# Performance work log

Hardware: AMD Instinct MI355X
Metric: run time of the kernel (lower is better)

## Reference

```python
import jax, jax.numpy as jnp
import numpy as np

E, K, H, I = 8, 2, 1024, 3584  # num_experts, top_k, hidden, intermediate


def setup_inputs() -> dict:
    key = jax.random.key(0)
    k0, k1, k2, k3, k4 = jax.random.split(key, 5)
    scale = 0.02
    return {
        "hidden_states": jax.random.normal(k0, (2, 1024, H), dtype=jnp.float32),
        "w_gate": jax.random.normal(k1, (E, H), dtype=jnp.float32) * scale,  # gate Linear H->E
        "w1": jax.random.normal(k2, (E, I, H), dtype=jnp.float32) * scale,   # gate proj
        "w3": jax.random.normal(k3, (E, I, H), dtype=jnp.float32) * scale,   # up proj
        "w2": jax.random.normal(k4, (E, H, I), dtype=jnp.float32) * scale,   # down proj
    }


def reference(hidden_states, w_gate, w1, w3, w2):
    B, S, Hd = hidden_states.shape
    x = hidden_states.reshape(-1, Hd)                       # [T, H]
    logits = jnp.einsum('th,eh->te', x, w_gate)             # router logits [T, E]
    probs = jax.nn.softmax(logits, axis=-1)
    topw, topi = jax.lax.top_k(probs, K)                    # [T, K]
    topw = topw / jnp.sum(topw, axis=-1, keepdims=True)     # renormalize=True
    # dense combine weights [T, E] (zero off the top-k)
    comb = jnp.sum(jax.nn.one_hot(topi, E, dtype=x.dtype) * topw[..., None], axis=1)
    # SwiGLU experts (dense reference over all experts; math matches dispatch+combine)
    g = jnp.einsum('th,eih->eti', x, w1)                    # [E, T, I]
    u = jnp.einsum('th,eih->eti', x, w3)
    h = jax.nn.silu(g) * u
    out = jnp.einsum('eti,ehi->eth', h, w2)                 # [E, T, H]
    y = jnp.einsum('te,eth->th', comb, out)                 # weighted combine
    return y.reshape(B, S, Hd)
```

## Files before the change

kernel.cpp:

```cpp
#include <hip/hip_runtime.h>
#include <hip/hip_bf16.h>
#include <stdint.h>

#define NEXP 8
#define HD 1024
#define ID 3584
#define NTOK 2048
#define NSLOT 4096
#define SLOT_PAD 128
#define NSLOT_ALLOC (NSLOT + SLOT_PAD)
#define WN (NEXP * ID * HD)
#define KSPLIT 4
#define KLEN (ID / KSPLIT)

typedef unsigned short u16;
typedef __attribute__((ext_vector_type(8))) short s16x8;
typedef __attribute__((ext_vector_type(4))) short s16x4;
typedef __attribute__((ext_vector_type(4))) float f32x4;

__device__ __forceinline__ u16 f2bf(float f) {
    __hip_bfloat16 h = __float2bfloat16(f);
    union { __hip_bfloat16 h; u16 u; } v; v.h = h; return v.u;
}

__device__ __forceinline__ s16x8 cvt8(f32x4 a, f32x4 b) {
    s16x8 o;
    o[0]=(short)f2bf(a[0]); o[1]=(short)f2bf(a[1]); o[2]=(short)f2bf(a[2]); o[3]=(short)f2bf(a[3]);
    o[4]=(short)f2bf(b[0]); o[5]=(short)f2bf(b[1]); o[6]=(short)f2bf(b[2]); o[7]=(short)f2bf(b[3]);
    return o;
}

__device__ __forceinline__ void glds16(const void* g, void* l) {
    __builtin_amdgcn_global_load_lds((const __attribute__((address_space(1))) unsigned*)g,
                                     (__attribute__((address_space(3))) unsigned*)l, 16, 0, 0);
}

__global__ void init_kernel(int* __restrict__ counts) {
    if (threadIdx.x < 16) counts[threadIdx.x] = 0;
}

__global__ void router_kernel(const float* __restrict__ x, const float* __restrict__ wg,
                              int* __restrict__ topk_idx, float* __restrict__ topk_w,
                              int* __restrict__ counts) {
    int t = blockIdx.x;
    int lane = threadIdx.x;
    const float* xr = x + (size_t)t * HD;
    float acc[NEXP];
#pragma unroll
    for (int e = 0; e < NEXP; ++e) acc[e] = 0.f;
#pragma unroll
    for (int i = 0; i < HD / 256; ++i) {
        int h = i * 256 + lane * 4;
        f32x4 xv = *(const f32x4*)(xr + h);
#pragma unroll
        for (int e = 0; e < NEXP; ++e) {
            f32x4 wv = *(const f32x4*)(wg + e * HD + h);
            acc[e] += xv[0]*wv[0] + xv[1]*wv[1] + xv[2]*wv[2] + xv[3]*wv[3];
        }
    }
#pragma unroll
    for (int e = 0; e < NEXP; ++e) {
#pragma unroll
        for (int s = 32; s > 0; s >>= 1) acc[e] += __shfl_xor(acc[e], s, 64);
    }
    if (lane == 0) {
        int b0 = 0; float l0 = acc[0];
#pragma unroll
        for (int e = 1; e < NEXP; ++e) if (acc[e] > l0) { l0 = acc[e]; b0 = e; }
        int b1 = (b0 == 0) ? 1 : 0; float l1 = acc[b1];
#pragma unroll
        for (int e = 0; e < NEXP; ++e) {
            if (e == b0 || e == b1) continue;
            if (acc[e] > l1) { l1 = acc[e]; b1 = e; }
        }
        float w0 = 1.f / (1.f + expf(l1 - l0));
        float w1 = 1.f - w0;
        topk_idx[2 * t] = b0; topk_idx[2 * t + 1] = b1;
        topk_w[2 * t] = w0;  topk_w[2 * t + 1] = w1;
        atomicAdd(&counts[b0], 1);
        atomicAdd(&counts[b1], 1);
    }
}

__global__ void scan_kernel(const int* __restrict__ counts, int* __restrict__ offsets,
                            int* __restrict__ rows) {
    if (threadIdx.x == 0) {
        int off = 0;
#pragma unroll
        for (int e = 0; e < NEXP; ++e) { offsets[e] = off; off += counts[e]; }
    }
    if (threadIdx.x < SLOT_PAD) rows[NSLOT + threadIdx.x] = 0;
}

__global__ void assign_kernel(const int* __restrict__ topk_idx, const int* __restrict__ offsets,
                              int* __restrict__ counts2, int* __restrict__ rows,
                              int* __restrict__ slot_of) {
    int i = blockIdx.x * 256 + threadIdx.x;
    int e = topk_idx[i];
    int pos = atomicAdd(&counts2[e], 1);
    int slot = offsets[e] + pos;
    rows[slot] = i >> 1;
    slot_of[i] = slot;
}

__global__ __launch_bounds__(256)
void cvt3_kernel(const float* __restrict__ x, u16* __restrict__ xbf,
                 const float* __restrict__ w1, u16* __restrict__ w1bf,
                 const float* __restrict__ w3, u16* __restrict__ w3bf) {
    const int NX = NTOK * HD / 8, NW = WN / 8;
    int stride = gridDim.x * 256;
    for (int i = blockIdx.x * 256 + threadIdx.x; i < NX + 2 * NW; i += stride) {
        const float* s; u16* d; int j;
        if (i < NX)            { s = x;  d = xbf;  j = i; }
        else if (i < NX + NW)  { s = w1; d = w1bf; j = i - NX; }
        else                   { s = w3; d = w3bf; j = i - NX - NW; }
        f32x4 v0 = ((const f32x4*)s)[2 * j];
        f32x4 v1 = ((const f32x4*)s)[2 * j + 1];
        ((s16x8*)d)[j] = cvt8(v0, v1);
    }
}

#define G1_BLOCKS (NEXP * (NTOK / 128) * (ID / 128))
#define CVT2_BLOCKS 1024
__global__ __launch_bounds__(256, 2)
void gemm1_kernel(const u16* __restrict__ xbf, const u16* __restrict__ w1bf,
                  const u16* __restrict__ w3bf, const int* __restrict__ counts,
                  const int* __restrict__ offsets, const int* __restrict__ rows,
                  u16* __restrict__ hbuf,
                  const float* __restrict__ w2, u16* __restrict__ w2bf) {
    __shared__ u16 As[128][32];
    __shared__ u16 B1s[128][32];
    __shared__ u16 B3s[128][32];

    if (blockIdx.x >= G1_BLOCKS) {
        const int stride = CVT2_BLOCKS * 256;
        for (int i = (blockIdx.x - G1_BLOCKS) * 256 + threadIdx.x; i < WN / 8; i += stride) {
            f32x4 v0 = ((const f32x4*)w2)[2 * i];
            f32x4 v1 = ((const f32x4*)w2)[2 * i + 1];
            ((s16x8*)w2bf)[i] = cvt8(v0, v1);
        }
        return;
    }

    int bid = blockIdx.x;
    int gq = bid >> 7;
    int rm = bid & 127;
    int mt = rm >> 3;
    int g  = gq * 8 + (rm & 7);
    int e  = g / 28;
    int nt = g - e * 28;

    int n_e = counts[e];
    int m0 = mt * 128;
    if (m0 >= n_e) return;
    int off = offsets[e];
    int n0 = nt * 128;

    int tid = threadIdx.x;
    int lane = tid & 63;
    int wid = tid >> 6;

    int srow = wid * 32 + (lane >> 2);
    int chunk = ((lane & 3) ^ ((srow >> 1) & 3)) * 8;

    int tokA0 = rows[off + m0 + srow];
    int tokA1 = rows[off + m0 + srow + 16];
    const u16* srcA0 = xbf + (size_t)tokA0 * HD + chunk;
    const u16* srcA1 = xbf + (size_t)tokA1 * HD + chunk;
    const u16* srcB1a = w1bf + ((size_t)e * ID + n0 + srow) * HD + chunk;
    const u16* srcB1b = srcB1a + (size_t)16 * HD;
    const u16* srcB3a = w3bf + ((size_t)e * ID + n0 + srow) * HD + chunk;
    const u16* srcB3b = srcB3a + (size_t)16 * HD;

    f32x4 accg[4][4] = {}, accu[4][4] = {};
    int wm = (wid >> 1) * 64, wn = (wid & 1) * 64;
    int lr = lane & 15;
    int k8sw = ((lane >> 4) ^ ((lr >> 1) & 3)) * 8;

    for (int k0 = 0; k0 < HD; k0 += 32) {
        glds16(srcA0 + k0,  &As[wid * 32][0]);
        glds16(srcA1 + k0,  &As[wid * 32 + 16][0]);
        glds16(srcB1a + k0, &B1s[wid * 32][0]);
        glds16(srcB1b + k0, &B1s[wid * 32 + 16][0]);
        glds16(srcB3a + k0, &B3s[wid * 32][0]);
        glds16(srcB3b + k0, &B3s[wid * 32 + 16][0]);
        __syncthreads();
        s16x8 a[4], b1[4], b3[4];
#pragma unroll
        for (int f = 0; f < 4; ++f) {
            a[f]  = *(const s16x8*)&As[wm + f * 16 + lr][k8sw];
            b1[f] = *(const s16x8*)&B1s[wn + f * 16 + lr][k8sw];
            b3[f] = *(const s16x8*)&B3s[wn + f * 16 + lr][k8sw];
        }
#pragma unroll
        for (int fm = 0; fm < 4; ++fm)
#pragma unroll
            for (int fn = 0; fn < 4; ++fn) {
                accg[fm][fn] = __builtin_amdgcn_mfma_f32_16x16x32_bf16(a[fm], b1[fn], accg[fm][fn], 0, 0, 0);
                accu[fm][fn] = __builtin_amdgcn_mfma_f32_16x16x32_bf16(a[fm], b3[fn], accu[fm][fn], 0, 0, 0);
            }
        __syncthreads();
    }

    int lc = lane & 15;
    int lr4 = (lane >> 4) * 4;
#pragma unroll
    for (int fm = 0; fm < 4; ++fm) {
#pragma unroll
        for (int r = 0; r < 4; ++r) {
            int row = wm + fm * 16 + lr4 + r;
            if (m0 + row < n_e) {
                size_t base = (size_t)(off + m0 + row) * ID + n0 + wn;
#pragma unroll
                for (int fn = 0; fn < 4; ++fn) {
                    float g2 = accg[fm][fn][r];
                    float u = accu[fm][fn][r];
                    float hv = g2 * u / (1.f + expf(-g2));
                    hbuf[base + fn * 16 + lc] = f2bf(hv);
                }
            }
        }
    }
}

__global__ __launch_bounds__(256, 2)
void gemm2_kernel(const u16* __restrict__ hbuf, const u16* __restrict__ w2bf,
                  const int* __restrict__ counts, const int* __restrict__ offsets,
                  float* __restrict__ out2) {
    int bid = blockIdx.x;
    int e = bid & 7;
    int inner = bid >> 3;
    int mt = inner >> 5;
    int r2 = inner & 31;
    int nt = r2 >> 2;
    int ks = r2 & 3;

    int n_e = counts[e];
    int m0 = mt * 128;
    if (m0 >= n_e) return;
    int off = offsets[e];
    int n0 = nt * 128;
    int kbase = ks * KLEN;

    __shared__ u16 As[128][32];
    __shared__ u16 Bs[128][32];

    int tid = threadIdx.x;
    int lane = tid & 63;
    int wid = tid >> 6;

    int srow = wid * 32 + (lane >> 2);
    int chunk = ((lane & 3) ^ ((srow >> 1) & 3)) * 8;
    const u16* srcA0 = hbuf + (size_t)(off + m0 + srow) * ID + kbase + chunk;
    const u16* srcA1 = srcA0 + (size_t)16 * ID;
    const u16* srcB0 = w2bf + ((size_t)e * HD + n0 + srow) * ID + kbase + chunk;
    const u16* srcB1 = srcB0 + (size_t)16 * ID;

    f32x4 acc[4][4] = {};
    int wm = (wid >> 1) * 64, wn = (wid & 1) * 64;
    int lr = lane & 15;
    int k8sw = ((lane >> 4) ^ ((lr >> 1) & 3)) * 8;

    for (int k0 = 0; k0 < KLEN; k0 += 32) {
        glds16(srcA0 + k0, &As[wid * 32][0]);
        glds16(srcA1 + k0, &As[wid * 32 + 16][0]);
        glds16(srcB0 + k0, &Bs[wid * 32][0]);
        glds16(srcB1 + k0, &Bs[wid * 32 + 16][0]);
        __syncthreads();
        s16x8 a[4], b[4];
#pragma unroll
        for (int f = 0; f < 4; ++f) {
            a[f] = *(const s16x8*)&As[wm + f * 16 + lr][k8sw];
            b[f] = *(const s16x8*)&Bs[wn + f * 16 + lr][k8sw];
        }
#pragma unroll
        for (int fm = 0; fm < 4; ++fm)
#pragma unroll
            for (int fn = 0; fn < 4; ++fn)
                acc[fm][fn] = __builtin_amdgcn_mfma_f32_16x16x32_bf16(a[fm], b[fn], acc[fm][fn], 0, 0, 0);
        __syncthreads();
    }

    float* outp = out2 + (size_t)ks * NSLOT_ALLOC * HD;
    int lc = lane & 15;
    int lr4 = (lane >> 4) * 4;
#pragma unroll
    for (int fm = 0; fm < 4; ++fm) {
#pragma unroll
        for (int r = 0; r < 4; ++r) {
            int row = wm + fm * 16 + lr4 + r;
            if (m0 + row < n_e) {
                float* dst = outp + (size_t)(off + m0 + row) * HD + n0 + wn;
#pragma unroll
                for (int fn = 0; fn < 4; ++fn)
                    dst[fn * 16 + lc] = acc[fm][fn][r];
            }
        }
    }
}

__global__ void combine_kernel(const float* __restrict__ out2, const int* __restrict__ slot_of,
                               const float* __restrict__ topk_w, float* __restrict__ y) {
    int i = blockIdx.x * 256 + threadIdx.x;
    int t = i >> 8;
    int c = i & 255;
    int s0 = slot_of[2 * t], s1 = slot_of[2 * t + 1];
    float w0 = topk_w[2 * t], w1 = topk_w[2 * t + 1];
    f32x4 o = {0.f, 0.f, 0.f, 0.f};
#pragma unroll
    for (int ks = 0; ks < KSPLIT; ++ks) {
        const float* p = out2 + (size_t)ks * NSLOT_ALLOC * HD;
        f32x4 a = ((const f32x4*)(p + (size_t)s0 * HD))[c];
        f32x4 b = ((const f32x4*)(p + (size_t)s1 * HD))[c];
#pragma unroll
        for (int j = 0; j < 4; ++j) o[j] += w0 * a[j] + w1 * b[j];
    }
    ((f32x4*)(y + (size_t)t * HD))[c] = o;
}

extern "C" void kernel_launch(void* const* d_in, const int* in_sizes, int n_in,
                              void* d_out, int out_size, void* d_ws, size_t ws_size,
                              hipStream_t stream) {
    (void)in_sizes; (void)n_in; (void)out_size; (void)ws_size;
    const float* x  = (const float*)d_in[0];
    const float* wg = (const float*)d_in[1];
    const float* w1 = (const float*)d_in[2];
    const float* w3 = (const float*)d_in[3];
    const float* w2 = (const float*)d_in[4];
    float* y = (float*)d_out;

    char* ws = (char*)d_ws;
    int*   counts   = (int*)(ws + 0);
    int*   counts2  = (int*)(ws + 32);
    int*   offsets  = (int*)(ws + 64);
    int*   topk_idx = (int*)(ws + 128);
    float* topk_w   = (float*)(ws + 128 + (size_t)NSLOT * 4);
    int*   rows     = (int*)(ws + 128 + (size_t)NSLOT * 8);
    int*   slot_of  = (int*)(ws + 128 + (size_t)NSLOT * 8 + (size_t)NSLOT_ALLOC * 4);
    size_t off_xbf = 128 + (size_t)NSLOT * 12 + (size_t)NSLOT_ALLOC * 4;
    off_xbf = (off_xbf + 255) & ~(size_t)255;
    u16* xbf = (u16*)(ws + off_xbf);
    size_t off_h = off_xbf + (size_t)NTOK * HD * 2;
    u16* hbuf = (u16*)(ws + off_h);
    size_t off_w1 = off_h + (size_t)NSLOT_ALLOC * ID * 2;
    u16* w1bf = (u16*)(ws + off_w1);
    size_t off_w3 = off_w1 + (size_t)WN * 2;
    u16* w3bf = (u16*)(ws + off_w3);
    size_t off_w2 = off_w3 + (size_t)WN * 2;
    u16* w2bf = (u16*)(ws + off_w2);
    size_t off_o2 = off_w2 + (size_t)WN * 2;
    float* out2 = (float*)(ws + off_o2);

    init_kernel<<<1, 64, 0, stream>>>(counts);
    router_kernel<<<NTOK, 64, 0, stream>>>(x, wg, topk_idx, topk_w, counts);
    scan_kernel<<<1, 128, 0, stream>>>(counts, offsets, rows);
    assign_kernel<<<NSLOT / 256, 256, 0, stream>>>(topk_idx, offsets, counts2, rows, slot_of);
    cvt3_kernel<<<4096, 256, 0, stream>>>(x, xbf, w1, w1bf, w3, w3bf);
    gemm1_kernel<<<G1_BLOCKS + CVT2_BLOCKS, 256, 0, stream>>>(xbf, w1bf, w3bf, counts, offsets, rows, hbuf, w2, w2bf);
    gemm2_kernel<<<NEXP * (NTOK / 128) * (HD / 128) * KSPLIT, 256, 0, stream>>>(hbuf, w2bf, counts, offsets, out2);
    combine_kernel<<<(NTOK * HD / 4) / 256, 256, 0, stream>>>(out2, slot_of, topk_w, y);
}
```

Baseline: 345.2 us.

## Double K-tile depth to 64 in both expert GEMMs with 8-way XOR swizzle

Raises the K step of each LDS tile from 32 to 64 in gemm1 and gemm2. Each stage now issues four 16-byte global-to-LDS loads per row group and runs two MFMA sub-steps per sync, with the swizzle changed to an 8-chunk XOR pattern. The aim is to halve the number of barriers and loop iterations per tile and amortize load latency. The cost is double the LDS per block, which may reduce occupancy, especially for gemm1 with its three tiles. Slot padding and scan block size are also raised to keep the rows array consistent with the new loading pattern.

```diff
diff --git a/kernel.cpp b/kernel.cpp
--- a/kernel.cpp
+++ b/kernel.cpp
@@ -7,7 +7,7 @@
 #define ID 3584
 #define NTOK 2048
 #define NSLOT 4096
-#define SLOT_PAD 128
+#define SLOT_PAD 256
 #define NSLOT_ALLOC (NSLOT + SLOT_PAD)
 #define WN (NEXP * ID * HD)
 #define KSPLIT 4
@@ -128,9 +128,9 @@
                   const int* __restrict__ offsets, const int* __restrict__ rows,
                   u16* __restrict__ hbuf,
                   const float* __restrict__ w2, u16* __restrict__ w2bf) {
-    __shared__ u16 As[128][32];
-    __shared__ u16 B1s[128][32];
-    __shared__ u16 B3s[128][32];
+    __shared__ u16 As[128][64];
+    __shared__ u16 B1s[128][64];
+    __shared__ u16 B3s[128][64];
 
     if (blockIdx.x >= G1_BLOCKS) {
         const int stride = CVT2_BLOCKS * 256;
@@ -160,37 +160,54 @@
     int lane = tid & 63;
     int wid = tid >> 6;
 
-    int srow = wid * 32 + (lane >> 2);
-    int chunk = ((lane & 3) ^ ((srow >> 1) & 3)) * 8;
-
-    int tokA0 = rows[off + m0 + srow];
-    int tokA1 = rows[off + m0 + srow + 16];
-    const u16* srcA0 = xbf + (size_t)tokA0 * HD + chunk;
-    const u16* srcA1 = xbf + (size_t)tokA1 * HD + chunk;
-    const u16* srcB1a = w1bf + ((size_t)e * ID + n0 + srow) * HD + chunk;
-    const u16* srcB1b = srcB1a + (size_t)16 * HD;
-    const u16* srcB3a = w3bf + ((size_t)e * ID + n0 + srow) * HD + chunk;
-    const u16* srcB3b = srcB3a + (size_t)16 * HD;
+    int rsub = lane >> 3;
+    int chunk = ((lane & 7) ^ rsub) * 8;
+    int srow = wid * 32 + rsub;
+
+    const u16 *srcA[4], *srcB1[4], *srcB3[4];
+#pragma unroll
+    for (int j = 0; j < 4; ++j) {
+        int rl = srow + 8 * j;
+        int tok = rows[off + m0 + rl];
+        srcA[j]  = xbf  + (size_t)tok * HD + chunk;
+        srcB1[j] = w1bf + ((size_t)e * ID + n0 + rl) * HD + chunk;
+        srcB3[j] = w3bf + ((size_t)e * ID + n0 + rl) * HD + chunk;
+    }
 
     f32x4 accg[4][4] = {}, accu[4][4] = {};
     int wm = (wid >> 1) * 64, wn = (wid & 1) * 64;
     int lr = lane & 15;
-    int k8sw = ((lane >> 4) ^ ((lr >> 1) & 3)) * 8;
-
-    for (int k0 = 0; k0 < HD; k0 += 32) {
-        glds16(srcA0 + k0,  &As[wid * 32][0]);
-        glds16(srcA1 + k0,  &As[wid * 32 + 16][0]);
-        glds16(srcB1a + k0, &B1s[wid * 32][0]);
-        glds16(srcB1b + k0, &B1s[wid * 32 + 16][0]);
-        glds16(srcB3a + k0, &B3s[wid * 32][0]);
-        glds16(srcB3b + k0, &B3s[wid * 32 + 16][0]);
+    int kk = lane >> 4;
+    int ks0 = ((kk)     ^ (lr & 7)) * 8;
+    int ks1 = ((4 + kk) ^ (lr & 7)) * 8;
+
+    for (int k0 = 0; k0 < HD; k0 += 64) {
+#pragma unroll
+        for (int j = 0; j < 4; ++j) {
+            glds16(srcA[j]  + k0, &As[wid * 32 + 8 * j][0]);
+            glds16(srcB1[j] + k0, &B1s[wid * 32 + 8 * j][0]);
+            glds16(srcB3[j] + k0, &B3s[wid * 32 + 8 * j][0]);
+        }
         __syncthreads();
         s16x8 a[4], b1[4], b3[4];
 #pragma unroll
         for (int f = 0; f < 4; ++f) {
-            a[f]  = *(const s16x8*)&As[wm + f * 16 + lr][k8sw];
-            b1[f] = *(const s16x8*)&B1s[wn + f * 16 + lr][k8sw];
-            b3[f] = *(const s16x8*)&B3s[wn + f * 16 + lr][k8sw];
+            a[f]  = *(const s16x8*)&As[wm + f * 16 + lr][ks0];
+            b1[f] = *(const s16x8*)&B1s[wn + f * 16 + lr][ks0];
+            b3[f] = *(const s16x8*)&B3s[wn + f * 16 + lr][ks0];
+        }
+#pragma unroll
+        for (int fm = 0; fm < 4; ++fm)
+#pragma unroll
+            for (int fn = 0; fn < 4; ++fn) {
+                accg[fm][fn] = __builtin_amdgcn_mfma_f32_16x16x32_bf16(a[fm], b1[fn], accg[fm][fn], 0, 0, 0);
+                accu[fm][fn] = __builtin_amdgcn_mfma_f32_16x16x32_bf16(a[fm], b3[fn], accu[fm][fn], 0, 0, 0);
+            }
+#pragma unroll
+        for (int f = 0; f < 4; ++f) {
+            a[f]  = *(const s16x8*)&As[wm + f * 16 + lr][ks1];
+            b1[f] = *(const s16x8*)&B1s[wn + f * 16 + lr][ks1];
+            b3[f] = *(const s16x8*)&B3s[wn + f * 16 + lr][ks1];
         }
 #pragma unroll
         for (int fm = 0; fm < 4; ++fm)
@@ -242,36 +259,54 @@
     int n0 = nt * 128;
     int kbase = ks * KLEN;
 
-    __shared__ u16 As[128][32];
-    __shared__ u16 Bs[128][32];
+    __shared__ u16 As[128][64];
+    __shared__ u16 Bs[128][64];
 
     int tid = threadIdx.x;
     int lane = tid & 63;
     int wid = tid >> 6;
 
-    int srow = wid * 32 + (lane >> 2);
-    int chunk = ((lane & 3) ^ ((srow >> 1) & 3)) * 8;
-    const u16* srcA0 = hbuf + (size_t)(off + m0 + srow) * ID + kbase + chunk;
-    const u16* srcA1 = srcA0 + (size_t)16 * ID;
-    const u16* srcB0 = w2bf + ((size_t)e * HD + n0 + srow) * ID + kbase + chunk;
-    const u16* srcB1 = srcB0 + (size_t)16 * ID;
+    int rsub = lane >> 3;
+    int chunk = ((lane & 7) ^ rsub) * 8;
+    int srow = wid * 32 + rsub;
+
+    const u16 *srcA[4], *srcB[4];
+#pragma unroll
+    for (int j = 0; j < 4; ++j) {
+        int rl = srow + 8 * j;
+        srcA[j] = hbuf + (size_t)(off + m0 + rl) * ID + kbase + chunk;
+        srcB[j] = w2bf + ((size_t)e * HD + n0 + rl) * ID + kbase + chunk;
+    }
 
     f32x4 acc[4][4] = {};
     int wm = (wid >> 1) * 64, wn = (wid & 1) * 64;
     int lr = lane & 15;
-    int k8sw = ((lane >> 4) ^ ((lr >> 1) & 3)) * 8;
-
-    for (int k0 = 0; k0 < KLEN; k0 += 32) {
-        glds16(srcA0 + k0, &As[wid * 32][0]);
-        glds16(srcA1 + k0, &As[wid * 32 + 16][0]);
-        glds16(srcB0 + k0, &Bs[wid * 32][0]);
-        glds16(srcB1 + k0, &Bs[wid * 32 + 16][0]);
+    int kk = lane >> 4;
+    int ks0 = ((kk)     ^ (lr & 7)) * 8;
+    int ks1 = ((4 + kk) ^ (lr & 7)) * 8;
+
+    for (int k0 = 0; k0 < KLEN; k0 += 64) {
+#pragma unroll
+        for (int j = 0; j < 4; ++j) {
+            glds16(srcA[j] + k0, &As[wid * 32 + 8 * j][0]);
+            glds16(srcB[j] + k0, &Bs[wid * 32 + 8 * j][0]);
+        }
         __syncthreads();
         s16x8 a[4], b[4];
 #pragma unroll
         for (int f = 0; f < 4; ++f) {
-            a[f] = *(const s16x8*)&As[wm + f * 16 + lr][k8sw];
-            b[f] = *(const s16x8*)&Bs[wn + f * 16 + lr][k8sw];
+            a[f] = *(const s16x8*)&As[wm + f * 16 + lr][ks0];
+            b[f] = *(const s16x8*)&Bs[wn + f * 16 + lr][ks0];
+        }
+#pragma unroll
+        for (int fm = 0; fm < 4; ++fm)
+#pragma unroll
+            for (int fn = 0; fn < 4; ++fn)
+                acc[fm][fn] = __builtin_amdgcn_mfma_f32_16x16x32_bf16(a[fm], b[fn], acc[fm][fn], 0, 0, 0);
+#pragma unroll
+        for (int f = 0; f < 4; ++f) {
+            a[f] = *(const s16x8*)&As[wm + f * 16 + lr][ks1];
+            b[f] = *(const s16x8*)&Bs[wn + f * 16 + lr][ks1];
         }
 #pragma unroll
         for (int fm = 0; fm < 4; ++fm)
@@ -353,7 +388,7 @@
 
     init_kernel<<<1, 64, 0, stream>>>(counts);
     router_kernel<<<NTOK, 64, 0, stream>>>(x, wg, topk_idx, topk_w, counts);
-    scan_kernel<<<1, 128, 0, stream>>>(counts, offsets, rows);
+    scan_kernel<<<1, 256, 0, stream>>>(counts, offsets, rows);
     assign_kernel<<<NSLOT / 256, 256, 0, stream>>>(topk_idx, offsets, counts2, rows, slot_of);
     cvt3_kernel<<<4096, 256, 0, stream>>>(x, xbf, w1, w1bf, w3, w3bf);
     gemm1_kernel<<<G1_BLOCKS + CVT2_BLOCKS, 256, 0, stream>>>(xbf, w1bf, w3bf, counts, offsets, rows, hbuf, w2, w2bf);
```

Result: no change. 341.2 us (-1.2%).
